# Kernel optimization log

Measured on AMD Instinct MI355X. Metric: run time of the kernel, lower is better.

Reference implementation:

```python
import jax, jax.numpy as jnp
import numpy as np

NEG_INF_SCALE = -1e9  # matches mask * -1000000000.0 in the original


def setup_inputs() -> dict:
    key = jax.random.key(0)
    k1, k2, k3, k4 = jax.random.split(key, 4)
    B, H, S, D = 2, 16, 2048, 64
    return {
        "query": jax.random.normal(k1, (B, H, S, D), dtype=jnp.float32),
        "key": jax.random.normal(k2, (B, H, S, D), dtype=jnp.float32),
        "value": jax.random.normal(k3, (B, H, S, D), dtype=jnp.float32),
        "mask": jax.random.randint(k4, (B, 1, 1, S), 0, 2, dtype=jnp.int32),
    }


def reference(query, key, value, mask):
    head_dimension = query.shape[-1]
    scale = 1.0 / jnp.sqrt(jnp.float32(head_dimension))
    # (b h q d),(b h k d) -> (b h q k)
    logits = jnp.einsum("bhqd,bhkd->bhqk", query, key) * scale
    logits = logits + mask.astype(logits.dtype) * NEG_INF_SCALE
    attention_weights = jax.nn.softmax(logits, axis=-1)
    # (b h q k),(b h k d) -> (b h q d)
    output = jnp.einsum("bhqk,bhkd->bhqd", attention_weights, value)
    return output, attention_weights
```

## Files before the change

### kernel.cpp

```cpp
#include <hip/hip_runtime.h>

#define SEQ   2048
#define DIM   64
#define NB    2
#define NH    16
#define NHEAD (NB * NH)
#define BQ    128
#define BK    64
#define NKT   (SEQ / BK)
#define NQT   (SEQ / BQ)
#define QSCALE 0.18033688011112042f

typedef float  f32x4  __attribute__((ext_vector_type(4)));
typedef short  bf16x8 __attribute__((ext_vector_type(8)));
typedef short  s16x4  __attribute__((ext_vector_type(4)));
typedef unsigned short u16;
typedef u16    u16x8  __attribute__((ext_vector_type(8)));
typedef unsigned int u32x4 __attribute__((ext_vector_type(4)));

__device__ __forceinline__ short f2bf(float x) {
    unsigned u = __float_as_uint(x);
    return (short)((u + 0x7FFFu + ((u >> 16) & 1u)) >> 16);
}

__device__ __forceinline__ unsigned cvtpk(float lo, float hi) {
    unsigned r;
    asm("v_cvt_pk_bf16_f32 %0, %1, %2" : "=v"(r) : "v"(lo), "v"(hi));
    return r;
}

__device__ __forceinline__ void gll16(const void* g, void* l) {
    __builtin_amdgcn_global_load_lds(
        (const __attribute__((address_space(1))) unsigned int*)g,
        (__attribute__((address_space(3))) unsigned int*)l, 16, 0, 0);
}

__device__ __forceinline__ bf16x8 ldfrag_swz(const u16* tile, int row, int kbase) {
    const char* rp = (const char*)(tile + row * 64);
    const int sw = (row & 7) << 4;
    s16x4 lo = *reinterpret_cast<const s16x4*>(rp + (((kbase << 1)     ) ^ sw));
    s16x4 hi = *reinterpret_cast<const s16x4*>(rp + (((kbase << 1) + 32) ^ sw));
    bf16x8 f;
    f[0] = lo[0]; f[1] = lo[1]; f[2] = lo[2]; f[3] = lo[3];
    f[4] = hi[0]; f[5] = hi[1]; f[6] = hi[2]; f[7] = hi[3];
    return f;
}

__global__ __launch_bounds__(256)
void conv_k_kernel(const float* __restrict__ K, u16* __restrict__ Kp)
{
    const int idx = (int)blockIdx.x * 256 + (int)threadIdx.x;
    const int u  = idx & 7;
    const int r  = (idx >> 3) & 63;
    const int kt = (idx >> 9) & 31;
    const int h  = idx >> 14;
    const int d0 = ((u ^ (r & 7)) << 3);
    const float* src = K + (((size_t)h * SEQ + (size_t)kt * 64 + r) * DIM + d0);
    const float4 a = *reinterpret_cast<const float4*>(src);
    const float4 b = *reinterpret_cast<const float4*>(src + 4);
    u16x8 o;
    o[0] = (u16)f2bf(a.x); o[1] = (u16)f2bf(a.y); o[2] = (u16)f2bf(a.z); o[3] = (u16)f2bf(a.w);
    o[4] = (u16)f2bf(b.x); o[5] = (u16)f2bf(b.y); o[6] = (u16)f2bf(b.z); o[7] = (u16)f2bf(b.w);
    *reinterpret_cast<u16x8*>(Kp + (size_t)idx * 8) = o;
}

__global__ __launch_bounds__(256)
void conv_v_kernel(const float* __restrict__ V, u16* __restrict__ Vp)
{
    __shared__ float tile[64][65];
    const int tid = (int)threadIdx.x;
    const int h   = (int)blockIdx.x >> 5;
    const int kt  = (int)blockIdx.x & 31;

    const int row0 = tid >> 4;
    const int c0   = (tid & 15) << 2;
    #pragma unroll
    for (int i = 0; i < 4; ++i) {
        const int row = row0 + (i << 4);
        const float4 v = *reinterpret_cast<const float4*>(
            V + (((size_t)h * SEQ + (size_t)kt * 64 + row) * DIM + c0));
        tile[row][c0 + 0] = v.x; tile[row][c0 + 1] = v.y;
        tile[row][c0 + 2] = v.z; tile[row][c0 + 3] = v.w;
    }
    __syncthreads();

    #pragma unroll
    for (int i = 0; i < 2; ++i) {
        const int oi = tid + i * 256;
        const int u  = oi & 7;
        const int rd = oi >> 3;
        const int k0 = ((u ^ (rd & 7)) << 3);
        u16x8 o;
        #pragma unroll
        for (int j = 0; j < 8; ++j)
            o[j] = (u16)f2bf(tile[k0 + j][rd]);
        *reinterpret_cast<u16x8*>(Vp + ((size_t)((h * 32 + kt) * 512 + oi)) * 8) = o;
    }
}

__global__ __launch_bounds__(512, 4)
void sdpa_main_kernel(const float* __restrict__ Qp, const u16* __restrict__ Kp,
                      const u16* __restrict__ Vp, const int* __restrict__ Mp,
                      float* __restrict__ Op, float* __restrict__ Pg_)
{
    __shared__ u16   Ks[3][4096];
    __shared__ u16   Vs[3][4096];
    __shared__ float Fb[SEQ];

    const int tid  = (int)threadIdx.x;
    const int lane = tid & 63;
    const int w    = tid >> 6;
    const int mrow = lane & 15;
    const int kgrp = (lane >> 4) << 2;

    const int bid  = (int)blockIdx.x;
    const int xcd  = bid & 7;
    const int slot = bid >> 3;
    const int bh   = xcd * 4 + (slot >> 4);
    const int qt   = slot & 15;

    const size_t headoff = (size_t)bh * SEQ * DIM;
    const float* Qg = Qp + headoff + (size_t)qt * BQ * DIM;
    const u16*   Kh = Kp + (size_t)bh * NKT * 4096;
    const u16*   Vh = Vp + (size_t)bh * NKT * 4096;
    const int*   Mg = Mp + (size_t)(bh / NH) * SEQ;
    float*       Og = Op + headoff + (size_t)qt * BQ * DIM;
    float*       Pg = Pg_ + ((size_t)bh * SEQ + (size_t)qt * BQ) * SEQ;

    {
        const int4 m0 = *reinterpret_cast<const int4*>(Mg + tid * 4);
        float4 f0;
        f0.x = m0.x ? -1.0e9f : 0.0f; f0.y = m0.y ? -1.0e9f : 0.0f;
        f0.z = m0.z ? -1.0e9f : 0.0f; f0.w = m0.w ? -1.0e9f : 0.0f;
        *reinterpret_cast<float4*>(&Fb[tid * 4]) = f0;
    }

    bf16x8 qf0, qf1;
    {
        const float* qrow = Qg + (size_t)(w * 16 + mrow) * DIM;
        const float4 a = *reinterpret_cast<const float4*>(qrow + kgrp);
        const float4 b = *reinterpret_cast<const float4*>(qrow + 16 + kgrp);
        const float4 c = *reinterpret_cast<const float4*>(qrow + 32 + kgrp);
        const float4 d = *reinterpret_cast<const float4*>(qrow + 48 + kgrp);
        qf0[0] = f2bf(a.x * QSCALE); qf0[1] = f2bf(a.y * QSCALE);
        qf0[2] = f2bf(a.z * QSCALE); qf0[3] = f2bf(a.w * QSCALE);
        qf0[4] = f2bf(b.x * QSCALE); qf0[5] = f2bf(b.y * QSCALE);
        qf0[6] = f2bf(b.z * QSCALE); qf0[7] = f2bf(b.w * QSCALE);
        qf1[0] = f2bf(c.x * QSCALE); qf1[1] = f2bf(c.y * QSCALE);
        qf1[2] = f2bf(c.z * QSCALE); qf1[3] = f2bf(c.w * QSCALE);
        qf1[4] = f2bf(d.x * QSCALE); qf1[5] = f2bf(d.y * QSCALE);
        qf1[6] = f2bf(d.z * QSCALE); qf1[7] = f2bf(d.w * QSCALE);
    }
    __syncthreads();

    const int so = tid * 8;

    gll16(Kh + so, &Ks[0][so]);
    gll16(Kh + 4096 + so, &Ks[1][so]);

    float lsum = 0.f;
    int bcur = 0, bpre = 2;

    for (int kt = 0; kt < NKT; ++kt) {
        asm volatile("s_waitcnt vmcnt(1)" ::: "memory");
        __builtin_amdgcn_s_barrier();
        gll16(Kh + (size_t)((kt + 2) & (NKT - 1)) * 4096 + so, &Ks[bpre][so]);
        __builtin_amdgcn_sched_barrier(0);

        const int k0 = kt * BK;
        #pragma unroll
        for (int t = 0; t < 4; ++t) {
            const bf16x8 kf0 = ldfrag_swz(Ks[bcur], t * 16 + mrow, kgrp);
            const bf16x8 kf1 = ldfrag_swz(Ks[bcur], t * 16 + mrow, 32 + kgrp);
            f32x4 a = {0.f, 0.f, 0.f, 0.f};
            a = __builtin_amdgcn_mfma_f32_16x16x32_bf16(kf0, qf0, a, 0, 0, 0);
            a = __builtin_amdgcn_mfma_f32_16x16x32_bf16(kf1, qf1, a, 0, 0, 0);
            const float4 b = *reinterpret_cast<const float4*>(&Fb[k0 + t * 16 + kgrp]);
            lsum += __builtin_amdgcn_exp2f(a[0] + b.x);
            lsum += __builtin_amdgcn_exp2f(a[1] + b.y);
            lsum += __builtin_amdgcn_exp2f(a[2] + b.z);
            lsum += __builtin_amdgcn_exp2f(a[3] + b.w);
        }

        bcur = (bcur == 2) ? 0 : bcur + 1;
        bpre = (bpre == 2) ? 0 : bpre + 1;
    }

    asm volatile("s_waitcnt vmcnt(0)" ::: "memory");

    lsum += __shfl_xor(lsum, 16);
    lsum += __shfl_xor(lsum, 32);
    const float rinv = 1.0f / lsum;

    __builtin_amdgcn_s_barrier();

    f32x4 oacc[4];
    #pragma unroll
    for (int n = 0; n < 4; ++n) {
        oacc[n][0] = 0.f; oacc[n][1] = 0.f; oacc[n][2] = 0.f; oacc[n][3] = 0.f;
    }

    gll16(Kh + so, &Ks[0][so]);
    gll16(Vh + so, &Vs[0][so]);
    gll16(Kh + 4096 + so, &Ks[1][so]);
    gll16(Vh + 4096 + so, &Vs[1][so]);
    asm volatile("s_waitcnt vmcnt(2)" ::: "memory");
    __builtin_amdgcn_s_barrier();
    bcur = 0; bpre = 2;

    float* prow = Pg + (size_t)(w * 16 + mrow) * SEQ + kgrp;

    for (int kt = 0; kt < NKT; ++kt) {
        if (kt == 1) { asm volatile("s_waitcnt vmcnt(6)" ::: "memory"); }
        else         { asm volatile("s_waitcnt vmcnt(10)" ::: "memory"); }
        __builtin_amdgcn_s_barrier();
        {
            const size_t nt = (size_t)((kt + 2) & (NKT - 1)) * 4096;
            gll16(Kh + nt + so, &Ks[bpre][so]);
            gll16(Vh + nt + so, &Vs[bpre][so]);
        }
        __builtin_amdgcn_sched_barrier(0);

        const int k0 = kt * BK;
        bf16x8 pf0, pf1;

        #pragma unroll
        for (int half = 0; half < 2; ++half) {
            f32x4 p[2];
            #pragma unroll
            for (int i = 0; i < 2; ++i) {
                const int t = half * 2 + i;
                const bf16x8 kf0 = ldfrag_swz(Ks[bcur], t * 16 + mrow, kgrp);
                const bf16x8 kf1 = ldfrag_swz(Ks[bcur], t * 16 + mrow, 32 + kgrp);
                f32x4 a = {0.f, 0.f, 0.f, 0.f};
                a = __builtin_amdgcn_mfma_f32_16x16x32_bf16(kf0, qf0, a, 0, 0, 0);
                a = __builtin_amdgcn_mfma_f32_16x16x32_bf16(kf1, qf1, a, 0, 0, 0);
                const float4 b = *reinterpret_cast<const float4*>(&Fb[k0 + t * 16 + kgrp]);
                p[i][0] = __builtin_amdgcn_exp2f(a[0] + b.x) * rinv;
                p[i][1] = __builtin_amdgcn_exp2f(a[1] + b.y) * rinv;
                p[i][2] = __builtin_amdgcn_exp2f(a[2] + b.z) * rinv;
                p[i][3] = __builtin_amdgcn_exp2f(a[3] + b.w) * rinv;
                *reinterpret_cast<float4*>(prow + k0 + t * 16) =
                    *reinterpret_cast<const float4*>(&p[i]);
            }
            const u32x4 packed = { cvtpk(p[0][0], p[0][1]), cvtpk(p[0][2], p[0][3]),
                                   cvtpk(p[1][0], p[1][1]), cvtpk(p[1][2], p[1][3]) };
            if (half == 0) pf0 = __builtin_bit_cast(bf16x8, packed);
            else           pf1 = __builtin_bit_cast(bf16x8, packed);
        }

        #pragma unroll
        for (int n = 0; n < 4; ++n) {
            const bf16x8 vf0 = ldfrag_swz(Vs[bcur], n * 16 + mrow, kgrp);
            const bf16x8 vf1 = ldfrag_swz(Vs[bcur], n * 16 + mrow, 32 + kgrp);
            oacc[n] = __builtin_amdgcn_mfma_f32_16x16x32_bf16(pf0, vf0, oacc[n], 0, 0, 0);
            oacc[n] = __builtin_amdgcn_mfma_f32_16x16x32_bf16(pf1, vf1, oacc[n], 0, 0, 0);
        }

        bcur = (bcur == 2) ? 0 : bcur + 1;
        bpre = (bpre == 2) ? 0 : bpre + 1;
    }

    #pragma unroll
    for (int n = 0; n < 4; ++n) {
        #pragma unroll
        for (int r = 0; r < 4; ++r)
            Og[(size_t)(w * 16 + kgrp + r) * DIM + n * 16 + mrow] = oacc[n][r];
    }
}

extern "C" void kernel_launch(void* const* d_in, const int* in_sizes, int n_in,
                              void* d_out, int out_size, void* d_ws, size_t ws_size,
                              hipStream_t stream) {
    const float* Q = (const float*)d_in[0];
    const float* K = (const float*)d_in[1];
    const float* V = (const float*)d_in[2];
    const int*   M = (const int*)d_in[3];
    float* O = (float*)d_out;
    float* P = O + (size_t)NB * NH * SEQ * DIM;

    u16* Kp = (u16*)d_ws;
    u16* Vp = Kp + (size_t)NHEAD * SEQ * DIM;

    conv_k_kernel<<<dim3(NHEAD * NKT * 64 * 8 / 256), dim3(256), 0, stream>>>(K, Kp);
    conv_v_kernel<<<dim3(NHEAD * NKT), dim3(256), 0, stream>>>(V, Vp);

    sdpa_main_kernel<<<dim3(NHEAD * NQT), dim3(512, 1, 1), 0, stream>>>(Q, Kp, Vp, M, O, P);
}
```

Before: 189.5 us.

## Pre-arrange K/V in MFMA fragment order for single 16-byte LDS reads

The conversion kernels now write K and V in bf16 directly in the per-lane MFMA fragment order. Each lane in the main kernel can then fetch a fragment with one contiguous 16-byte LDS load, replacing two swizzled 8-byte loads plus index arithmetic. The V conversion drops its shared-memory transpose and reads strided global scalars instead, so that pre-pass may become less coalesced. The main kernel's inner loops issue fewer LDS instructions, and the new layout should stay bank-conflict free because each lane reads consecutive 16-byte chunks.

Result: no change. 191.8 us (+1.2%).

```diff
diff --git a/kernel.cpp b/kernel.cpp
--- a/kernel.cpp
+++ b/kernel.cpp
@@ -13,7 +13,6 @@
 
 typedef float  f32x4  __attribute__((ext_vector_type(4)));
 typedef short  bf16x8 __attribute__((ext_vector_type(8)));
-typedef short  s16x4  __attribute__((ext_vector_type(4)));
 typedef unsigned short u16;
 typedef u16    u16x8  __attribute__((ext_vector_type(8)));
 typedef unsigned int u32x4 __attribute__((ext_vector_type(4)));
@@ -35,29 +34,22 @@
         (__attribute__((address_space(3))) unsigned int*)l, 16, 0, 0);
 }
 
-__device__ __forceinline__ bf16x8 ldfrag_swz(const u16* tile, int row, int kbase) {
-    const char* rp = (const char*)(tile + row * 64);
-    const int sw = (row & 7) << 4;
-    s16x4 lo = *reinterpret_cast<const s16x4*>(rp + (((kbase << 1)     ) ^ sw));
-    s16x4 hi = *reinterpret_cast<const s16x4*>(rp + (((kbase << 1) + 32) ^ sw));
-    bf16x8 f;
-    f[0] = lo[0]; f[1] = lo[1]; f[2] = lo[2]; f[3] = lo[3];
-    f[4] = hi[0]; f[5] = hi[1]; f[6] = hi[2]; f[7] = hi[3];
-    return f;
-}
-
 __global__ __launch_bounds__(256)
 void conv_k_kernel(const float* __restrict__ K, u16* __restrict__ Kp)
 {
-    const int idx = (int)blockIdx.x * 256 + (int)threadIdx.x;
-    const int u  = idx & 7;
-    const int r  = (idx >> 3) & 63;
-    const int kt = (idx >> 9) & 31;
-    const int h  = idx >> 14;
-    const int d0 = ((u ^ (r & 7)) << 3);
-    const float* src = K + (((size_t)h * SEQ + (size_t)kt * 64 + r) * DIM + d0);
+    const int idx  = (int)blockIdx.x * 256 + (int)threadIdx.x;
+    const int lane = idx & 63;
+    const int s    = (idx >> 6) & 7;
+    const int kt   = (idx >> 9) & 31;
+    const int h    = idx >> 14;
+    const int mrow = lane & 15;
+    const int kg4  = (lane >> 4) << 2;
+    const int row  = (s >> 1) * 16 + mrow;
+    const int cb   = (s & 1) * 32 + kg4;
+
+    const float* src = K + ((size_t)h * SEQ + (size_t)kt * 64 + row) * DIM + cb;
     const float4 a = *reinterpret_cast<const float4*>(src);
-    const float4 b = *reinterpret_cast<const float4*>(src + 4);
+    const float4 b = *reinterpret_cast<const float4*>(src + 16);
     u16x8 o;
     o[0] = (u16)f2bf(a.x); o[1] = (u16)f2bf(a.y); o[2] = (u16)f2bf(a.z); o[3] = (u16)f2bf(a.w);
     o[4] = (u16)f2bf(b.x); o[5] = (u16)f2bf(b.y); o[6] = (u16)f2bf(b.z); o[7] = (u16)f2bf(b.w);
@@ -67,35 +59,24 @@
 __global__ __launch_bounds__(256)
 void conv_v_kernel(const float* __restrict__ V, u16* __restrict__ Vp)
 {
-    __shared__ float tile[64][65];
-    const int tid = (int)threadIdx.x;
-    const int h   = (int)blockIdx.x >> 5;
-    const int kt  = (int)blockIdx.x & 31;
-
-    const int row0 = tid >> 4;
-    const int c0   = (tid & 15) << 2;
+    const int idx  = (int)blockIdx.x * 256 + (int)threadIdx.x;
+    const int lane = idx & 63;
+    const int s    = (idx >> 6) & 7;
+    const int kt   = (idx >> 9) & 31;
+    const int h    = idx >> 14;
+    const int mrow = lane & 15;
+    const int kg4  = (lane >> 4) << 2;
+    const int rd   = (s >> 1) * 16 + mrow;
+    const int cb   = (s & 1) * 32 + kg4;
+
+    const float* vb = V + ((size_t)h * SEQ + (size_t)kt * 64) * DIM;
+    u16x8 o;
     #pragma unroll
-    for (int i = 0; i < 4; ++i) {
-        const int row = row0 + (i << 4);
-        const float4 v = *reinterpret_cast<const float4*>(
-            V + (((size_t)h * SEQ + (size_t)kt * 64 + row) * DIM + c0));
-        tile[row][c0 + 0] = v.x; tile[row][c0 + 1] = v.y;
-        tile[row][c0 + 2] = v.z; tile[row][c0 + 3] = v.w;
-    }
-    __syncthreads();
-
-    #pragma unroll
-    for (int i = 0; i < 2; ++i) {
-        const int oi = tid + i * 256;
-        const int u  = oi & 7;
-        const int rd = oi >> 3;
-        const int k0 = ((u ^ (rd & 7)) << 3);
-        u16x8 o;
-        #pragma unroll
-        for (int j = 0; j < 8; ++j)
-            o[j] = (u16)f2bf(tile[k0 + j][rd]);
-        *reinterpret_cast<u16x8*>(Vp + ((size_t)((h * 32 + kt) * 512 + oi)) * 8) = o;
-    }
+    for (int j = 0; j < 4; ++j) {
+        o[j]     = (u16)f2bf(vb[(size_t)(cb + j) * DIM + rd]);
+        o[4 + j] = (u16)f2bf(vb[(size_t)(cb + 16 + j) * DIM + rd]);
+    }
+    *reinterpret_cast<u16x8*>(Vp + (size_t)idx * 8) = o;
 }
 
 __global__ __launch_bounds__(512, 4)
@@ -111,7 +92,7 @@
     const int lane = tid & 63;
     const int w    = tid >> 6;
     const int mrow = lane & 15;
-    const int kgrp = (lane >> 4) << 2;
+    const int kg4  = (lane >> 4) << 2;
 
     const int bid  = (int)blockIdx.x;
     const int xcd  = bid & 7;
@@ -138,10 +119,10 @@
     bf16x8 qf0, qf1;
     {
         const float* qrow = Qg + (size_t)(w * 16 + mrow) * DIM;
-        const float4 a = *reinterpret_cast<const float4*>(qrow + kgrp);
-        const float4 b = *reinterpret_cast<const float4*>(qrow + 16 + kgrp);
-        const float4 c = *reinterpret_cast<const float4*>(qrow + 32 + kgrp);
-        const float4 d = *reinterpret_cast<const float4*>(qrow + 48 + kgrp);
+        const float4 a = *reinterpret_cast<const float4*>(qrow + kg4);
+        const float4 b = *reinterpret_cast<const float4*>(qrow + 16 + kg4);
+        const float4 c = *reinterpret_cast<const float4*>(qrow + 32 + kg4);
+        const float4 d = *reinterpret_cast<const float4*>(qrow + 48 + kg4);
         qf0[0] = f2bf(a.x * QSCALE); qf0[1] = f2bf(a.y * QSCALE);
         qf0[2] = f2bf(a.z * QSCALE); qf0[3] = f2bf(a.w * QSCALE);
         qf0[4] = f2bf(b.x * QSCALE); qf0[5] = f2bf(b.y * QSCALE);
@@ -153,7 +134,8 @@
     }
     __syncthreads();
 
-    const int so = tid * 8;
+    const int so  = tid * 8;
+    const int lo8 = lane * 8;
 
     gll16(Kh + so, &Ks[0][so]);
     gll16(Kh + 4096 + so, &Ks[1][so]);
@@ -167,15 +149,16 @@
         gll16(Kh + (size_t)((kt + 2) & (NKT - 1)) * 4096 + so, &Ks[bpre][so]);
         __builtin_amdgcn_sched_barrier(0);
 
+        const u16* kp = &Ks[bcur][lo8];
         const int k0 = kt * BK;
         #pragma unroll
         for (int t = 0; t < 4; ++t) {
-            const bf16x8 kf0 = ldfrag_swz(Ks[bcur], t * 16 + mrow, kgrp);
-            const bf16x8 kf1 = ldfrag_swz(Ks[bcur], t * 16 + mrow, 32 + kgrp);
+            const bf16x8 kf0 = *reinterpret_cast<const bf16x8*>(kp + (2 * t) * 512);
+            const bf16x8 kf1 = *reinterpret_cast<const bf16x8*>(kp + (2 * t + 1) * 512);
             f32x4 a = {0.f, 0.f, 0.f, 0.f};
             a = __builtin_amdgcn_mfma_f32_16x16x32_bf16(kf0, qf0, a, 0, 0, 0);
             a = __builtin_amdgcn_mfma_f32_16x16x32_bf16(kf1, qf1, a, 0, 0, 0);
-            const float4 b = *reinterpret_cast<const float4*>(&Fb[k0 + t * 16 + kgrp]);
+            const float4 b = *reinterpret_cast<const float4*>(&Fb[k0 + t * 16 + kg4]);
             lsum += __builtin_amdgcn_exp2f(a[0] + b.x);
             lsum += __builtin_amdgcn_exp2f(a[1] + b.y);
             lsum += __builtin_amdgcn_exp2f(a[2] + b.z);
@@ -208,7 +191,7 @@
     __builtin_amdgcn_s_barrier();
     bcur = 0; bpre = 2;
 
-    float* prow = Pg + (size_t)(w * 16 + mrow) * SEQ + kgrp;
+    float* prow = Pg + (size_t)(w * 16 + mrow) * SEQ + kg4;
 
     for (int kt = 0; kt < NKT; ++kt) {
         if (kt == 1) { asm volatile("s_waitcnt vmcnt(6)" ::: "memory"); }
@@ -221,6 +204,8 @@
         }
         __builtin_amdgcn_sched_barrier(0);
 
+        const u16* kp = &Ks[bcur][lo8];
+        const u16* vp = &Vs[bcur][lo8];
         const int k0 = kt * BK;
         bf16x8 pf0, pf1;
 
@@ -230,12 +215,12 @@
             #pragma unroll
             for (int i = 0; i < 2; ++i) {
                 const int t = half * 2 + i;
-                const bf16x8 kf0 = ldfrag_swz(Ks[bcur], t * 16 + mrow, kgrp);
-                const bf16x8 kf1 = ldfrag_swz(Ks[bcur], t * 16 + mrow, 32 + kgrp);
+                const bf16x8 kf0 = *reinterpret_cast<const bf16x8*>(kp + (2 * t) * 512);
+                const bf16x8 kf1 = *reinterpret_cast<const bf16x8*>(kp + (2 * t + 1) * 512);
                 f32x4 a = {0.f, 0.f, 0.f, 0.f};
                 a = __builtin_amdgcn_mfma_f32_16x16x32_bf16(kf0, qf0, a, 0, 0, 0);
                 a = __builtin_amdgcn_mfma_f32_16x16x32_bf16(kf1, qf1, a, 0, 0, 0);
-                const float4 b = *reinterpret_cast<const float4*>(&Fb[k0 + t * 16 + kgrp]);
+                const float4 b = *reinterpret_cast<const float4*>(&Fb[k0 + t * 16 + kg4]);
                 p[i][0] = __builtin_amdgcn_exp2f(a[0] + b.x) * rinv;
                 p[i][1] = __builtin_amdgcn_exp2f(a[1] + b.y) * rinv;
                 p[i][2] = __builtin_amdgcn_exp2f(a[2] + b.z) * rinv;
@@ -251,8 +236,8 @@
 
         #pragma unroll
         for (int n = 0; n < 4; ++n) {
-            const bf16x8 vf0 = ldfrag_swz(Vs[bcur], n * 16 + mrow, kgrp);
-            const bf16x8 vf1 = ldfrag_swz(Vs[bcur], n * 16 + mrow, 32 + kgrp);
+            const bf16x8 vf0 = *reinterpret_cast<const bf16x8*>(vp + (2 * n) * 512);
+            const bf16x8 vf1 = *reinterpret_cast<const bf16x8*>(vp + (2 * n + 1) * 512);
             oacc[n] = __builtin_amdgcn_mfma_f32_16x16x32_bf16(pf0, vf0, oacc[n], 0, 0, 0);
             oacc[n] = __builtin_amdgcn_mfma_f32_16x16x32_bf16(pf1, vf1, oacc[n], 0, 0, 0);
         }
@@ -265,7 +250,7 @@
     for (int n = 0; n < 4; ++n) {
         #pragma unroll
         for (int r = 0; r < 4; ++r)
-            Og[(size_t)(w * 16 + kgrp + r) * DIM + n * 16 + mrow] = oacc[n][r];
+            Og[(size_t)(w * 16 + kg4 + r) * DIM + n * 16 + mrow] = oacc[n][r];
     }
 }
 
@@ -282,8 +267,9 @@
     u16* Kp = (u16*)d_ws;
     u16* Vp = Kp + (size_t)NHEAD * SEQ * DIM;
 
-    conv_k_kernel<<<dim3(NHEAD * NKT * 64 * 8 / 256), dim3(256), 0, stream>>>(K, Kp);
-    conv_v_kernel<<<dim3(NHEAD * NKT), dim3(256), 0, stream>>>(V, Vp);
+    const int conv_blocks = NHEAD * NKT * 8 * 64 / 256;
+    conv_k_kernel<<<dim3(conv_blocks), dim3(256), 0, stream>>>(K, Kp);
+    conv_v_kernel<<<dim3(conv_blocks), dim3(256), 0, stream>>>(V, Vp);
 
     sdpa_main_kernel<<<dim3(NHEAD * NQT), dim3(512, 1, 1), 0, stream>>>(Q, Kp, Vp, M, O, P);
 }
```
